# Kernel tuning notes

Hardware: AMD Instinct MI355X
Metric: run time of the kernel (lower is better)

Reference implementation:

```python
import jax, jax.numpy as jnp
import numpy as np

T, B, E, H, V, K = 512, 64, 256, 512, 50000, 50
START, STOP = 0, K - 1  # tags = ['<START>'] + tags + ['<STOP>']


def setup_inputs() -> dict:
    key = jax.random.key(0)
    ks = jax.random.split(key, 13)
    p = lambda k, shape, s=0.02: jax.random.normal(k, shape, jnp.float32) * s
    return {
        'tokens': jax.random.randint(ks[0], (T, B), 0, V, dtype=jnp.int32),
        'embed': p(ks[1], (V, E), 0.1),
        'w_ih_f': p(ks[2], (4 * H, E)), 'w_hh_f': p(ks[3], (4 * H, H)), 'b_f': jnp.zeros((4 * H,), jnp.float32),
        'w_ih_b': p(ks[4], (4 * H, E)), 'w_hh_b': p(ks[5], (4 * H, H)), 'b_b': jnp.zeros((4 * H,), jnp.float32),
        'w_enc': p(ks[6], (H, 2 * H)), 'b_enc': jnp.zeros((H,), jnp.float32),
        'w_out': p(ks[7], (K, H)), 'b_out': jnp.zeros((K,), jnp.float32),
        'trans': p(ks[8], (K, K), 0.1),
    }


def _lstm_dir(x, w_ih, w_hh, b, reverse):
    # x: [T,B,E] -> hidden states [T,B,H]; torch gate order i,f,g,o
    bsz = x.shape[1]
    h_dim = w_hh.shape[1]
    xp = jnp.einsum('tbe,ge->tbg', x, w_ih) + b  # precompute input projections

    def step(carry, xt):
        h, c = carry
        g = xt + h @ w_hh.T
        i, f, gg, o = jnp.split(g, 4, axis=-1)
        c = jax.nn.sigmoid(f) * c + jax.nn.sigmoid(i) * jnp.tanh(gg)
        h = jax.nn.sigmoid(o) * jnp.tanh(c)
        return (h, c), h

    init = (jnp.zeros((bsz, h_dim), x.dtype), jnp.zeros((bsz, h_dim), x.dtype))
    _, hs = jax.lax.scan(step, init, xp, reverse=reverse)
    return hs


def reference(tokens, embed, w_ih_f, w_hh_f, b_f, w_ih_b, w_hh_b, b_b,
              w_enc, b_enc, w_out, b_out, trans):
    x = embed[tokens]  # [T,B,E]
    hf = _lstm_dir(x, w_ih_f, w_hh_f, b_f, reverse=False)
    hb = _lstm_dir(x, w_ih_b, w_hh_b, b_b, reverse=True)
    enc = jnp.concatenate([hf, hb], axis=-1)                      # [T,B,2H]
    states = jnp.tanh(jnp.einsum('tbd,hd->tbh', enc, w_enc) + b_enc)
    emit = jnp.einsum('tbh,kh->tbk', states, w_out) + b_out       # [T,B,K]

    # CRF forward algorithm (log partition). trans[j, i] = score of i -> j.
    NEG = jnp.float32(-10000.0)
    bsz, k = emit.shape[1], emit.shape[2]
    alpha0 = jnp.full((bsz, k), NEG).at[:, START].set(0.0)

    def crf_step(alpha, e_t):
        # scores[b, j, i] = alpha[b, i] + trans[j, i] + emit[b, t, j]
        s = alpha[:, None, :] + trans[None, :, :] + e_t[:, :, None]
        return jax.nn.logsumexp(s, axis=-1), None

    alpha, _ = jax.lax.scan(crf_step, alpha0, emit)
    log_z = jax.nn.logsumexp(alpha + trans[STOP][None, :], axis=-1)  # [B]
    return log_z
```

## Files before the change

### kernel.cpp

```cpp
#include <hip/hip_runtime.h>
#include <stdint.h>

#define T_ 512
#define B_ 64
#define E_ 256
#define H_ 512
#define KT 50

typedef __attribute__((ext_vector_type(8))) short bf16x8;
typedef __attribute__((ext_vector_type(4))) float f32x4;
typedef __attribute__((ext_vector_type(4))) int i32x4;

#define MFMA16(a,b,c) __builtin_amdgcn_mfma_f32_16x16x32_bf16((a),(b),(c),0,0,0)

static __device__ __forceinline__ float bf2f(unsigned short v) {
  unsigned int u = ((unsigned int)v) << 16; float f; __builtin_memcpy(&f, &u, 4); return f;
}
static __device__ __forceinline__ unsigned short f2bf(float f) {
  unsigned int u; __builtin_memcpy(&u, &f, 4);
  u += 0x7fffu + ((u >> 16) & 1u);
  return (unsigned short)(u >> 16);
}
static __device__ __forceinline__ float sigm(float x) { return 1.f / (1.f + __expf(-x)); }
static __device__ __forceinline__ float tanh_(float x) { return 2.f / (1.f + __expf(-2.f * x)) - 1.f; }

static __device__ __forceinline__ unsigned int load_dw_dev(const unsigned int* p) {
  unsigned int v;
  asm volatile("global_load_dword %0, %1, off sc0 sc1\n\ts_waitcnt vmcnt(0)"
               : "=v"(v) : "v"(p) : "memory");
  return v;
}

__global__ void probe_kernel(const unsigned short* __restrict__ e,
                             unsigned int* __restrict__ flag) {
  int lane = threadIdx.x & 63;
  float a = fabsf(bf2f(e[2 * lane]));
  int good = (a >= 1e-8f && a <= 4.0f);
  unsigned long long m = __ballot(good);
  if (threadIdx.x == 0) flag[0] = (__popcll(m) >= 48) ? 1u : 0u;
}

struct CvtArgs { const void* src; unsigned short* dst; int n; };
struct CvtPack { CvtArgs a[11]; };

__global__ __launch_bounds__(256) void convert_kernel(CvtPack p,
                                                      const unsigned int* __restrict__ flag) {
  CvtArgs c = p.a[blockIdx.y];
  int i = (blockIdx.x * 256 + threadIdx.x) * 8;
  if (i >= c.n) return;
  int isbf = *flag;
  if (i + 8 <= c.n) {
    if (isbf) {
      *(i32x4*)(c.dst + i) = *(const i32x4*)((const unsigned short*)c.src + i);
    } else {
      const float* s = (const float*)c.src;
      float4 a0 = *(const float4*)(s + i);
      float4 a1 = *(const float4*)(s + i + 4);
      unsigned short o[8] = {f2bf(a0.x), f2bf(a0.y), f2bf(a0.z), f2bf(a0.w),
                             f2bf(a1.x), f2bf(a1.y), f2bf(a1.z), f2bf(a1.w)};
      *(i32x4*)(c.dst + i) = *(i32x4*)o;
    }
  } else {
    for (int j = 0; j < 8; j++) {
      if (i + j < c.n) {
        c.dst[i + j] = isbf ? ((const unsigned short*)c.src)[i + j]
                            : f2bf(((const float*)c.src)[i + j]);
      }
    }
  }
}

__global__ __launch_bounds__(256) void embed_kernel(
    const int* __restrict__ tokens, const void* __restrict__ embed,
    const unsigned int* __restrict__ flag, unsigned short* __restrict__ x) {
  int tid = threadIdx.x;
  int row = blockIdx.x * 8 + (tid >> 5);
  int l = tid & 31;
  int tok = tokens[row];
  if (*flag) {
    const unsigned short* e = (const unsigned short*)embed;
    *(i32x4*)(x + (size_t)row * E_ + l * 8) =
        *(const i32x4*)(e + (size_t)tok * E_ + l * 8);
  } else {
    const float* e = (const float*)embed + (size_t)tok * E_ + l * 8;
    float4 a0 = *(const float4*)e;
    float4 a1 = *(const float4*)(e + 4);
    unsigned short o[8] = {f2bf(a0.x), f2bf(a0.y), f2bf(a0.z), f2bf(a0.w),
                           f2bf(a1.x), f2bf(a1.y), f2bf(a1.z), f2bf(a1.w)};
    *(i32x4*)(x + (size_t)row * E_ + l * 8) = *(i32x4*)o;
  }
}

__global__ __launch_bounds__(256, 1) void lstm_kernel(
    const unsigned short* __restrict__ whh_f, const unsigned short* __restrict__ wih_f,
    const unsigned short* __restrict__ bias_f,
    const unsigned short* __restrict__ whh_b, const unsigned short* __restrict__ wih_b,
    const unsigned short* __restrict__ bias_b,
    const unsigned short* __restrict__ x,
    unsigned short* __restrict__ hf, unsigned short* __restrict__ hb,
    unsigned int* __restrict__ tags) {
  const int tid = threadIdx.x;
  const int wv = tid >> 6, lane = tid & 63, q = lane >> 4, l15 = lane & 15;
  const int bid = blockIdx.x;
  const int dir = bid & 1;
  const int wg = bid >> 1;
  const int u0 = wg * 16;

  const unsigned short* whh = dir ? whh_b : whh_f;
  const unsigned short* wih = dir ? wih_b : wih_f;
  const unsigned short* bvec = dir ? bias_b : bias_f;
  unsigned short* hbuf = dir ? hb : hf;
  unsigned int* tbase = tags + (size_t)dir * 512;

  bf16x8 afrag[4][6];
#pragma unroll
  for (int mt = 0; mt < 4; mt++) {
    int row = mt * H_ + u0 + l15;
#pragma unroll
    for (int kl = 0; kl < 6; kl++) {
      const unsigned short* p = (kl < 4)
          ? (whh + (size_t)row * H_ + (wv * 4 + kl) * 32 + q * 8)
          : (wih + (size_t)row * E_ + (wv * 2 + (kl - 4)) * 32 + q * 8);
      afrag[mt][kl] = *(const bf16x8*)p;
    }
  }

  const int eb = tid & 63;
  const int uu = tid >> 6;
  float bg[4][4];
#pragma unroll
  for (int s = 0; s < 4; s++) {
    int u = uu + 4 * s;
#pragma unroll
    for (int g = 0; g < 4; g++) bg[s][g] = bf2f(bvec[g * H_ + u0 + u]);
  }
  float cst[4] = {0.f, 0.f, 0.f, 0.f};

  __shared__ float pacc[4][64][66];
  __shared__ __align__(16) unsigned short h_out[64][16];
  __shared__ unsigned int go_word;
  if (tid == 0) go_word = 0;

  for (int step = 0; step < T_; step++) {
    const int t = dir ? (T_ - 1 - step) : step;
    f32x4 acc[4][4];
#pragma unroll
    for (int mt = 0; mt < 4; mt++)
#pragma unroll
      for (int nt = 0; nt < 4; nt++) acc[mt][nt] = (f32x4){0.f, 0.f, 0.f, 0.f};

    {
      const unsigned short* xb = x + (size_t)t * B_ * E_;
#pragma unroll
      for (int kl = 4; kl < 6; kl++) {
        int ec = wv * 2 + (kl - 4);
#pragma unroll
        for (int nt = 0; nt < 4; nt++) {
          int b = nt * 16 + l15;
          bf16x8 bx = *(const bf16x8*)(xb + (size_t)b * E_ + ec * 32 + q * 8);
#pragma unroll
          for (int mt = 0; mt < 4; mt++)
            acc[mt][nt] = MFMA16(afrag[mt][kl], bx, acc[mt][nt]);
        }
      }
    }

    if (step > 0) {
      if (wv == 1) {
        const unsigned int* tp = tbase + (size_t)(lane & 31) * 16;
        for (;;) {
          unsigned int v = load_dw_dev(tp);
          unsigned long long m = __ballot((lane < 32) ? (v >= (unsigned)step) : 1);
          if (m == ~0ULL) break;
          __builtin_amdgcn_s_sleep(1);
        }
        __hip_atomic_store(&go_word, (unsigned int)step, __ATOMIC_RELAXED,
                           __HIP_MEMORY_SCOPE_WORKGROUP);
      } else {
        while (__hip_atomic_load(&go_word, __ATOMIC_RELAXED,
                                 __HIP_MEMORY_SCOPE_WORKGROUP) < (unsigned int)step)
          __builtin_amdgcn_s_sleep(1);
      }
      asm volatile("" ::: "memory");

      const int tprev = dir ? (t + 1) : (t - 1);
      const unsigned int* hD = (const unsigned int*)hbuf + (size_t)tprev * 16384;

      const unsigned int* a0 = hD + ((wv * 4 + 0) * 4 + q) * 256 + l15 * 4;
      const unsigned int* a1 = hD + ((wv * 4 + 1) * 4 + q) * 256 + l15 * 4;
      const unsigned int* a2 = hD + ((wv * 4 + 2) * 4 + q) * 256 + l15 * 4;
      const unsigned int* a3 = hD + ((wv * 4 + 3) * 4 + q) * 256 + l15 * 4;
      i32x4 h00, h01, h02, h03, h10, h11, h12, h13;
      i32x4 h20, h21, h22, h23, h30, h31, h32, h33;
      asm volatile(
          "global_load_dwordx4 %0, %16, off sc0 sc1\n\t"
          "global_load_dwordx4 %1, %16, off offset:1024 sc0 sc1\n\t"
          "global_load_dwordx4 %2, %16, off offset:2048 sc0 sc1\n\t"
          "global_load_dwordx4 %3, %16, off offset:3072 sc0 sc1\n\t"
          "global_load_dwordx4 %4, %17, off sc0 sc1\n\t"
          "global_load_dwordx4 %5, %17, off offset:1024 sc0 sc1\n\t"
          "global_load_dwordx4 %6, %17, off offset:2048 sc0 sc1\n\t"
          "global_load_dwordx4 %7, %17, off offset:3072 sc0 sc1\n\t"
          "global_load_dwordx4 %8, %18, off sc0 sc1\n\t"
          "global_load_dwordx4 %9, %18, off offset:1024 sc0 sc1\n\t"
          "global_load_dwordx4 %10, %18, off offset:2048 sc0 sc1\n\t"
          "global_load_dwordx4 %11, %18, off offset:3072 sc0 sc1\n\t"
          "global_load_dwordx4 %12, %19, off sc0 sc1\n\t"
          "global_load_dwordx4 %13, %19, off offset:1024 sc0 sc1\n\t"
          "global_load_dwordx4 %14, %19, off offset:2048 sc0 sc1\n\t"
          "global_load_dwordx4 %15, %19, off offset:3072 sc0 sc1\n\t"
          "s_waitcnt vmcnt(0)"
          : "=&v"(h00), "=&v"(h01), "=&v"(h02), "=&v"(h03),
            "=&v"(h10), "=&v"(h11), "=&v"(h12), "=&v"(h13),
            "=&v"(h20), "=&v"(h21), "=&v"(h22), "=&v"(h23),
            "=&v"(h30), "=&v"(h31), "=&v"(h32), "=&v"(h33)
          : "v"(a0), "v"(a1), "v"(a2), "v"(a3)
          : "memory");
      i32x4 hr4[16] = {h00, h01, h02, h03, h10, h11, h12, h13,
                       h20, h21, h22, h23, h30, h31, h32, h33};
#pragma unroll
      for (int kl = 0; kl < 4; kl++) {
#pragma unroll
        for (int nt = 0; nt < 4; nt++) {
          bf16x8 bh;
          __builtin_memcpy(&bh, &hr4[kl * 4 + nt], 16);
#pragma unroll
          for (int mt = 0; mt < 4; mt++)
            acc[mt][nt] = MFMA16(afrag[mt][kl], bh, acc[mt][nt]);
        }
      }
    }

    __syncthreads();
#pragma unroll
    for (int mt = 0; mt < 4; mt++)
#pragma unroll
      for (int nt = 0; nt < 4; nt++)
#pragma unroll
        for (int r = 0; r < 4; r++)
          pacc[wv][mt * 16 + q * 4 + r][nt * 16 + l15] = acc[mt][nt][r];
    __syncthreads();

#pragma unroll
    for (int s = 0; s < 4; s++) {
      int u = uu + 4 * s;
      float gi = bg[s][0], gf = bg[s][1], gg = bg[s][2], og = bg[s][3];
#pragma unroll
      for (int w = 0; w < 4; w++) {
        gi += pacc[w][u][eb];
        gf += pacc[w][16 + u][eb];
        gg += pacc[w][32 + u][eb];
        og += pacc[w][48 + u][eb];
      }
      float cn = sigm(gf) * cst[s] + sigm(gi) * tanh_(gg);
      cst[s] = cn;
      h_out[eb][u] = f2bf(sigm(og) * tanh_(cn));
    }
    __syncthreads();

    if (wv == 0) {
      unsigned int* gp = (unsigned int*)hbuf + (size_t)t * 16384 + wg * 512 + lane * 4;
      i32x4 v0 = *(const i32x4*)&h_out[lane][0];
      i32x4 v1 = *(const i32x4*)&h_out[lane][8];
      asm volatile(
          "global_store_dwordx4 %0, %1, off sc0 sc1\n\t"
          "global_store_dwordx4 %0, %2, off offset:1024 sc0 sc1\n\t"
          "s_waitcnt vmcnt(0)"
          :: "v"(gp), "v"(v0), "v"(v1) : "memory");
      if (lane == 0) {
        unsigned int* tp = tbase + (size_t)wg * 16;
        unsigned int tv = (unsigned int)(step + 1);
        asm volatile("global_store_dword %0, %1, off sc0 sc1"
                     :: "v"(tp), "v"(tv) : "memory");
      }
    }
  }
}

__global__ __launch_bounds__(256) void enc_kernel(
    const unsigned short* __restrict__ hf, const unsigned short* __restrict__ hb,
    const unsigned short* __restrict__ w_enc, const unsigned short* __restrict__ b_enc,
    unsigned short* __restrict__ states) {
  const int tid = threadIdx.x;
  const int bm = blockIdx.x, bn = blockIdx.y;
  const int wv = tid >> 6, lane = tid & 63, q = lane >> 4, l15 = lane & 15;
  const int wm = wv >> 1, wn = wv & 1;

  __shared__ __align__(16) unsigned short a_lds[128][72];
  __shared__ __align__(16) unsigned short b_lds[128][72];
  __shared__ __align__(16) unsigned short st_lds[128][136];

  f32x4 acc[4][4];
#pragma unroll
  for (int mt = 0; mt < 4; mt++)
#pragma unroll
    for (int nt = 0; nt < 4; nt++) acc[mt][nt] = (f32x4){0.f, 0.f, 0.f, 0.f};

  for (int c = 0; c < 16; c++) {
    const unsigned short* asrc = (c < 8) ? hf : hb;
    int kof = (c & 7) * 64;
#pragma unroll
    for (int p = 0; p < 4; p++) {
      int u_ = tid + p * 256;
      int r = u_ >> 3, wu = u_ & 7;
      int grow = bm * 128 + r;
      *(i32x4*)&a_lds[r][wu * 8] =
          *(const i32x4*)((const unsigned int*)asrc + (size_t)(grow >> 6) * 16384 +
                          (size_t)((kof >> 3) + wu) * 256 + (grow & 63) * 4);
      *(i32x4*)&b_lds[r][wu * 8] =
          *(const i32x4*)(w_enc + (size_t)(bn * 128 + r) * 1024 + c * 64 + wu * 8);
    }
    __syncthreads();
#pragma unroll
    for (int kk = 0; kk < 64; kk += 32) {
      bf16x8 af[4], bfr[4];
#pragma unroll
      for (int mt = 0; mt < 4; mt++)
        af[mt] = *(const bf16x8*)&a_lds[wm * 64 + mt * 16 + l15][kk + q * 8];
#pragma unroll
      for (int nt = 0; nt < 4; nt++)
        bfr[nt] = *(const bf16x8*)&b_lds[wn * 64 + nt * 16 + l15][kk + q * 8];
#pragma unroll
      for (int mt = 0; mt < 4; mt++)
#pragma unroll
        for (int nt = 0; nt < 4; nt++) acc[mt][nt] = MFMA16(af[mt], bfr[nt], acc[mt][nt]);
    }
    __syncthreads();
  }

  float be[4];
#pragma unroll
  for (int nt = 0; nt < 4; nt++)
    be[nt] = bf2f(b_enc[bn * 128 + wn * 64 + nt * 16 + l15]);
#pragma unroll
  for (int mt = 0; mt < 4; mt++)
#pragma unroll
    for (int nt = 0; nt < 4; nt++)
#pragma unroll
      for (int r = 0; r < 4; r++) {
        float v = tanh_(acc[mt][nt][r] + be[nt]);
        st_lds[wm * 64 + mt * 16 + q * 4 + r][wn * 64 + nt * 16 + l15] = f2bf(v);
      }
  __syncthreads();
#pragma unroll
  for (int p = 0; p < 8; p++) {
    int u_ = tid + p * 256;
    int r = u_ >> 4, w = u_ & 15;
    *(i32x4*)(states + (size_t)(bm * 128 + r) * H_ + bn * 128 + w * 8) =
        *(const i32x4*)&st_lds[r][w * 8];
  }
}

__global__ __launch_bounds__(256) void emit_kernel(
    const unsigned short* __restrict__ states, const unsigned short* __restrict__ w_out,
    const unsigned short* __restrict__ b_out, float* __restrict__ emit) {
  const int tid = threadIdx.x;
  const int bm = blockIdx.x;
  const int wv = tid >> 6, lane = tid & 63, q = lane >> 4, l15 = lane & 15;
  const int wm = wv >> 1, wn = wv & 1;

  __shared__ __align__(16) unsigned short wo_lds[64][520];
  __shared__ __align__(16) unsigned short a_lds[128][72];

#pragma unroll
  for (int p = 0; p < 16; p++) {
    int u = tid + p * 256;
    int r = u >> 6, wu = u & 63;
    i32x4 v = {0, 0, 0, 0};
    if (r < KT) v = *(const i32x4*)(w_out + (size_t)r * H_ + wu * 8);
    *(i32x4*)&wo_lds[r][wu * 8] = v;
  }

  f32x4 acc[4][2];
#pragma unroll
  for (int mt = 0; mt < 4; mt++)
#pragma unroll
    for (int nt = 0; nt < 2; nt++) acc[mt][nt] = (f32x4){0.f, 0.f, 0.f, 0.f};

  for (int c = 0; c < 8; c++) {
    __syncthreads();
#pragma unroll
    for (int p = 0; p < 4; p++) {
      int u = tid + p * 256;
      int r = u >> 3, wu = u & 7;
      *(i32x4*)&a_lds[r][wu * 8] =
          *(const i32x4*)(states + (size_t)(bm * 128 + r) * H_ + c * 64 + wu * 8);
    }
    __syncthreads();
#pragma unroll
    for (int kk = 0; kk < 64; kk += 32) {
      bf16x8 af[4], bfr[2];
#pragma unroll
      for (int mt = 0; mt < 4; mt++)
        af[mt] = *(const bf16x8*)&a_lds[wm * 64 + mt * 16 + l15][kk + q * 8];
#pragma unroll
      for (int nt = 0; nt < 2; nt++)
        bfr[nt] = *(const bf16x8*)&wo_lds[wn * 32 + nt * 16 + l15][c * 64 + kk + q * 8];
#pragma unroll
      for (int mt = 0; mt < 4; mt++)
#pragma unroll
        for (int nt = 0; nt < 2; nt++) acc[mt][nt] = MFMA16(af[mt], bfr[nt], acc[mt][nt]);
    }
  }

  float bo[2];
#pragma unroll
  for (int nt = 0; nt < 2; nt++) {
    int n = wn * 32 + nt * 16 + l15;
    bo[nt] = (n < KT) ? bf2f(b_out[n]) : 0.f;
  }
#pragma unroll
  for (int mt = 0; mt < 4; mt++)
#pragma unroll
    for (int nt = 0; nt < 2; nt++) {
      int n = wn * 32 + nt * 16 + l15;
      if (n < KT) {
#pragma unroll
        for (int r = 0; r < 4; r++) {
          int m = bm * 128 + wm * 64 + mt * 16 + q * 4 + r;
          emit[(size_t)m * KT + n] = acc[mt][nt][r] + bo[nt];
        }
      }
    }
}

__global__ __launch_bounds__(256) void crf_kernel(
    const float* __restrict__ emit, const unsigned short* __restrict__ trans,
    const unsigned int* __restrict__ flag, void* __restrict__ out) {
  const int tid = threadIdx.x;
  const int wv = tid >> 6, lane = tid & 63;
  const int b = blockIdx.x * 4 + wv;
  const int jj = (lane < KT) ? lane : (KT - 1);

  float tr[KT];
  float mj = -1e30f;
#pragma unroll
  for (int i = 0; i < KT; i++) {
    tr[i] = bf2f(trans[jj * KT + i]);
    mj = fmaxf(mj, tr[i]);
  }
  float et[KT];
#pragma unroll
  for (int i = 0; i < KT; i++) et[i] = __expf(tr[i] - mj);
  float tr_stop = bf2f(trans[(KT - 1) * KT + jj]);

  float alpha = (lane == 0) ? 0.f : -1e30f;
  float e_next = emit[(size_t)b * KT + jj];

  for (int t = 0; t < T_; t++) {
    float e_cur = e_next;
    if (t < T_ - 1) e_next = emit[((size_t)(t + 1) * B_ + b) * KT + jj];
    float M = alpha;
#pragma unroll
    for (int off = 32; off; off >>= 1) M = fmaxf(M, __shfl_xor(M, off, 64));
    float p = __expf(alpha - M);
    float s = 0.f;
#pragma unroll
    for (int i = 0; i < KT; i++) {
      float pi = __uint_as_float(__builtin_amdgcn_readlane(__float_as_uint(p), i));
      s = __builtin_fmaf(et[i], pi, s);
    }
    float an = e_cur + mj + M + __logf(s);
    alpha = (lane < KT) ? an : -1e30f;
  }

  float v = (lane < KT) ? (alpha + tr_stop) : -1e30f;
  float M2 = v;
#pragma unroll
  for (int off = 32; off; off >>= 1) M2 = fmaxf(M2, __shfl_xor(M2, off, 64));
  float s2 = (lane < KT) ? __expf(v - M2) : 0.f;
#pragma unroll
  for (int off = 32; off; off >>= 1) s2 += __shfl_xor(s2, off, 64);
  float lz = M2 + __logf(s2);
  if (lane == 0) {
    if (*flag) ((unsigned short*)out)[b] = f2bf(lz);
    else ((float*)out)[b] = lz;
  }
}

extern "C" void kernel_launch(void* const* d_in, const int* in_sizes, int n_in,
                              void* d_out, int out_size, void* d_ws, size_t ws_size,
                              hipStream_t stream) {
  const int* tokens = (const int*)d_in[0];
  const void* embed = d_in[1];
  const void* wih_f = d_in[2];
  const void* whh_f = d_in[3];
  const void* b_f = d_in[4];
  const void* wih_b = d_in[5];
  const void* whh_b = d_in[6];
  const void* b_b = d_in[7];
  const void* w_enc = d_in[8];
  const void* b_enc = d_in[9];
  const void* w_out = d_in[10];
  const void* b_out = d_in[11];
  const void* trans = d_in[12];

  char* ws = (char*)d_ws;
  unsigned int* tags = (unsigned int*)ws;
  unsigned int* pflag = (unsigned int*)(ws + 262144);
  unsigned short* xbuf = (unsigned short*)(ws + 262400);
  unsigned short* hf = (unsigned short*)(ws + 17039616);
  unsigned short* hb = (unsigned short*)(ws + 50594048);
  unsigned short* states = (unsigned short*)(ws + 84148480);
  float* emit = (float*)(ws + 117702912);
  unsigned short* canon = (unsigned short*)(ws + 124256512);

  unsigned short* c_wih_f = canon + 0;
  unsigned short* c_whh_f = canon + 524288;
  unsigned short* c_b_f   = canon + 1572864;
  unsigned short* c_wih_b = canon + 1574912;
  unsigned short* c_whh_b = canon + 2099200;
  unsigned short* c_b_b   = canon + 3147776;
  unsigned short* c_w_enc = canon + 3149824;
  unsigned short* c_b_enc = canon + 3674112;
  unsigned short* c_w_out = canon + 3674624;
  unsigned short* c_b_out = canon + 3700224;
  unsigned short* c_trans = canon + 3700352;

  hipMemsetAsync(tags, 0, 4096, stream);
  probe_kernel<<<1, 64, 0, stream>>>((const unsigned short*)embed, pflag);

  CvtPack pk;
  pk.a[0]  = {wih_f, c_wih_f, 524288};
  pk.a[1]  = {whh_f, c_whh_f, 1048576};
  pk.a[2]  = {b_f,   c_b_f,   2048};
  pk.a[3]  = {wih_b, c_wih_b, 524288};
  pk.a[4]  = {whh_b, c_whh_b, 1048576};
  pk.a[5]  = {b_b,   c_b_b,   2048};
  pk.a[6]  = {w_enc, c_w_enc, 524288};
  pk.a[7]  = {b_enc, c_b_enc, 512};
  pk.a[8]  = {w_out, c_w_out, 25600};
  pk.a[9]  = {b_out, c_b_out, 50};
  pk.a[10] = {trans, c_trans, 2500};
  convert_kernel<<<dim3(512, 11), 256, 0, stream>>>(pk, pflag);

  embed_kernel<<<(T_ * B_) / 8, 256, 0, stream>>>(tokens, embed, pflag, xbuf);
  lstm_kernel<<<64, 256, 0, stream>>>(c_whh_f, c_wih_f, c_b_f,
                                      c_whh_b, c_wih_b, c_b_b,
                                      xbuf, hf, hb, tags);
  enc_kernel<<<dim3(256, 4), 256, 0, stream>>>(hf, hb, c_w_enc, c_b_enc, states);
  emit_kernel<<<256, 256, 0, stream>>>(states, c_w_out, c_b_out, emit);
  crf_kernel<<<16, 256, 0, stream>>>(emit, c_trans, pflag, d_out);
}
```

Baseline: 2.789 ms.

## Pin each LSTM direction to one XCD and use L2-coherent sync

Launches 512 workgroups and reads the XCC_ID hardware register so that the first two XCDs to fill 32 workgroups each take one LSTM direction, and all other workgroups exit. A runtime probe then checks whether a store with sc0 only is visible to another workgroup in the same direction. If it is, the per-step hidden-state exchange and tag polling use sc0 loads and stores that stay in the shared L2 instead of sc1 system-coherent traffic. This is meant to cut inter-workgroup sync latency, at the cost of relying on undocumented dispatch behaviour and spinning workgroups during role assignment.

```diff
diff --git a/kernel.cpp b/kernel.cpp
--- a/kernel.cpp
+++ b/kernel.cpp
@@ -24,10 +24,14 @@
 static __device__ __forceinline__ float sigm(float x) { return 1.f / (1.f + __expf(-x)); }
 static __device__ __forceinline__ float tanh_(float x) { return 2.f / (1.f + __expf(-2.f * x)) - 1.f; }
 
-static __device__ __forceinline__ unsigned int load_dw_dev(const unsigned int* p) {
+static __device__ __forceinline__ unsigned int load_tag(const unsigned int* p, bool mall) {
   unsigned int v;
-  asm volatile("global_load_dword %0, %1, off sc0 sc1\n\ts_waitcnt vmcnt(0)"
-               : "=v"(v) : "v"(p) : "memory");
+  if (mall)
+    asm volatile("global_load_dword %0, %1, off sc0 sc1\n\ts_waitcnt vmcnt(0)"
+                 : "=v"(v) : "v"(p) : "memory");
+  else
+    asm volatile("global_load_dword %0, %1, off sc0\n\ts_waitcnt vmcnt(0)"
+                 : "=v"(v) : "v"(p) : "memory");
   return v;
 }
 
@@ -98,13 +102,54 @@
     const unsigned short* __restrict__ bias_b,
     const unsigned short* __restrict__ x,
     unsigned short* __restrict__ hf, unsigned short* __restrict__ hb,
-    unsigned int* __restrict__ tags) {
+    unsigned int* __restrict__ tags, unsigned int* __restrict__ ctrl) {
   const int tid = threadIdx.x;
+
+  __shared__ float pacc[4][64][66];
+  __shared__ __align__(16) unsigned short h_out[64][16];
+  __shared__ unsigned int lds_misc[3136];
+
+  if (tid == 0) {
+    unsigned int xcc;
+    asm volatile("s_getreg_b32 %0, hwreg(HW_REG_XCC_ID)" : "=s"(xcc));
+    xcc &= 15;
+    unsigned int slot = __hip_atomic_fetch_add(&ctrl[xcc], 1u, __ATOMIC_RELAXED,
+                                               __HIP_MEMORY_SCOPE_AGENT);
+    unsigned int role;
+    if (slot == 31) {
+      unsigned int r = __hip_atomic_fetch_add(&ctrl[16], 1u, __ATOMIC_RELAXED,
+                                              __HIP_MEMORY_SCOPE_AGENT);
+      role = (r < 2) ? (r + 1) : 3;
+      __hip_atomic_store(&ctrl[32 + xcc], role, __ATOMIC_RELAXED,
+                         __HIP_MEMORY_SCOPE_AGENT);
+      asm volatile("s_waitcnt vmcnt(0)" ::: "memory");
+      __hip_atomic_fetch_add(&ctrl[17], 1u, __ATOMIC_RELAXED,
+                             __HIP_MEMORY_SCOPE_AGENT);
+    } else {
+      for (;;) {
+        role = __hip_atomic_load(&ctrl[32 + xcc], __ATOMIC_RELAXED,
+                                 __HIP_MEMORY_SCOPE_AGENT);
+        if (role) break;
+        if (__hip_atomic_load(&ctrl[17], __ATOMIC_RELAXED,
+                              __HIP_MEMORY_SCOPE_AGENT) >= 2) {
+          role = __hip_atomic_load(&ctrl[32 + xcc], __ATOMIC_RELAXED,
+                                   __HIP_MEMORY_SCOPE_AGENT);
+          if (role == 0) role = 3;
+          break;
+        }
+        __builtin_amdgcn_s_sleep(8);
+      }
+    }
+    lds_misc[1] = role; lds_misc[2] = slot; lds_misc[0] = 0;
+  }
+  __syncthreads();
+  const unsigned int role = lds_misc[1];
+  const unsigned int wg = lds_misc[2];
+  if (role > 2 || wg >= 32) return;
+  const int dir = (int)role - 1;
+
   const int wv = tid >> 6, lane = tid & 63, q = lane >> 4, l15 = lane & 15;
-  const int bid = blockIdx.x;
-  const int dir = bid & 1;
-  const int wg = bid >> 1;
-  const int u0 = wg * 16;
+  const int u0 = (int)wg * 16;
 
   const unsigned short* whh = dir ? whh_b : whh_f;
   const unsigned short* wih = dir ? wih_b : wih_f;
@@ -136,10 +181,33 @@
   }
   float cst[4] = {0.f, 0.f, 0.f, 0.f};
 
-  __shared__ float pacc[4][64][66];
-  __shared__ __align__(16) unsigned short h_out[64][16];
-  __shared__ unsigned int go_word;
-  if (tid == 0) go_word = 0;
+  if (tid == 0) {
+    unsigned int* tw = ctrl + 64 + 32 * dir;
+    unsigned int* vw = ctrl + 128 + 32 * dir;
+    unsigned int sent = 0x5EED0001u + (unsigned)dir;
+    if (wg == 0) {
+      asm volatile("global_store_dword %0, %1, off sc0" :: "v"(tw), "v"(sent) : "memory");
+    } else if (wg == 1) {
+      unsigned int verdict = 1;
+      for (int it = 0; it < 4096; it++) {
+        unsigned int v;
+        asm volatile("global_load_dword %0, %1, off sc0\n\ts_waitcnt vmcnt(0)"
+                     : "=v"(v) : "v"(tw) : "memory");
+        if (v == sent) { verdict = 2; break; }
+        __builtin_amdgcn_s_sleep(1);
+      }
+      asm volatile("global_store_dword %0, %1, off sc0 sc1" :: "v"(vw), "v"(verdict) : "memory");
+    }
+    for (;;) {
+      unsigned int v;
+      asm volatile("global_load_dword %0, %1, off sc0 sc1\n\ts_waitcnt vmcnt(0)"
+                   : "=v"(v) : "v"(vw) : "memory");
+      if (v) { lds_misc[3] = v; break; }
+      __builtin_amdgcn_s_sleep(8);
+    }
+  }
+  __syncthreads();
+  const bool mall = (lds_misc[3] == 1u);
 
   for (int step = 0; step < T_; step++) {
     const int t = dir ? (T_ - 1 - step) : step;
@@ -169,15 +237,15 @@
       if (wv == 1) {
         const unsigned int* tp = tbase + (size_t)(lane & 31) * 16;
         for (;;) {
-          unsigned int v = load_dw_dev(tp);
+          unsigned int v = load_tag(tp, mall);
           unsigned long long m = __ballot((lane < 32) ? (v >= (unsigned)step) : 1);
           if (m == ~0ULL) break;
           __builtin_amdgcn_s_sleep(1);
         }
-        __hip_atomic_store(&go_word, (unsigned int)step, __ATOMIC_RELAXED,
+        __hip_atomic_store(&lds_misc[0], (unsigned int)step, __ATOMIC_RELAXED,
                            __HIP_MEMORY_SCOPE_WORKGROUP);
       } else {
-        while (__hip_atomic_load(&go_word, __ATOMIC_RELAXED,
+        while (__hip_atomic_load(&lds_misc[0], __ATOMIC_RELAXED,
                                  __HIP_MEMORY_SCOPE_WORKGROUP) < (unsigned int)step)
           __builtin_amdgcn_s_sleep(1);
       }
@@ -192,30 +260,57 @@
       const unsigned int* a3 = hD + ((wv * 4 + 3) * 4 + q) * 256 + l15 * 4;
       i32x4 h00, h01, h02, h03, h10, h11, h12, h13;
       i32x4 h20, h21, h22, h23, h30, h31, h32, h33;
-      asm volatile(
-          "global_load_dwordx4 %0, %16, off sc0 sc1\n\t"
-          "global_load_dwordx4 %1, %16, off offset:1024 sc0 sc1\n\t"
-          "global_load_dwordx4 %2, %16, off offset:2048 sc0 sc1\n\t"
-          "global_load_dwordx4 %3, %16, off offset:3072 sc0 sc1\n\t"
-          "global_load_dwordx4 %4, %17, off sc0 sc1\n\t"
-          "global_load_dwordx4 %5, %17, off offset:1024 sc0 sc1\n\t"
-          "global_load_dwordx4 %6, %17, off offset:2048 sc0 sc1\n\t"
-          "global_load_dwordx4 %7, %17, off offset:3072 sc0 sc1\n\t"
-          "global_load_dwordx4 %8, %18, off sc0 sc1\n\t"
-          "global_load_dwordx4 %9, %18, off offset:1024 sc0 sc1\n\t"
-          "global_load_dwordx4 %10, %18, off offset:2048 sc0 sc1\n\t"
-          "global_load_dwordx4 %11, %18, off offset:3072 sc0 sc1\n\t"
-          "global_load_dwordx4 %12, %19, off sc0 sc1\n\t"
-          "global_load_dwordx4 %13, %19, off offset:1024 sc0 sc1\n\t"
-          "global_load_dwordx4 %14, %19, off offset:2048 sc0 sc1\n\t"
-          "global_load_dwordx4 %15, %19, off offset:3072 sc0 sc1\n\t"
-          "s_waitcnt vmcnt(0)"
-          : "=&v"(h00), "=&v"(h01), "=&v"(h02), "=&v"(h03),
-            "=&v"(h10), "=&v"(h11), "=&v"(h12), "=&v"(h13),
-            "=&v"(h20), "=&v"(h21), "=&v"(h22), "=&v"(h23),
-            "=&v"(h30), "=&v"(h31), "=&v"(h32), "=&v"(h33)
-          : "v"(a0), "v"(a1), "v"(a2), "v"(a3)
-          : "memory");
+      if (mall) {
+        asm volatile(
+            "global_load_dwordx4 %0, %16, off sc0 sc1\n\t"
+            "global_load_dwordx4 %1, %16, off offset:1024 sc0 sc1\n\t"
+            "global_load_dwordx4 %2, %16, off offset:2048 sc0 sc1\n\t"
+            "global_load_dwordx4 %3, %16, off offset:3072 sc0 sc1\n\t"
+            "global_load_dwordx4 %4, %17, off sc0 sc1\n\t"
+            "global_load_dwordx4 %5, %17, off offset:1024 sc0 sc1\n\t"
+            "global_load_dwordx4 %6, %17, off offset:2048 sc0 sc1\n\t"
+            "global_load_dwordx4 %7, %17, off offset:3072 sc0 sc1\n\t"
+            "global_load_dwordx4 %8, %18, off sc0 sc1\n\t"
+            "global_load_dwordx4 %9, %18, off offset:1024 sc0 sc1\n\t"
+            "global_load_dwordx4 %10, %18, off offset:2048 sc0 sc1\n\t"
+            "global_load_dwordx4 %11, %18, off offset:3072 sc0 sc1\n\t"
+            "global_load_dwordx4 %12, %19, off sc0 sc1\n\t"
+            "global_load_dwordx4 %13, %19, off offset:1024 sc0 sc1\n\t"
+            "global_load_dwordx4 %14, %19, off offset:2048 sc0 sc1\n\t"
+            "global_load_dwordx4 %15, %19, off offset:3072 sc0 sc1\n\t"
+            "s_waitcnt vmcnt(0)"
+            : "=&v"(h00), "=&v"(h01), "=&v"(h02), "=&v"(h03),
+              "=&v"(h10), "=&v"(h11), "=&v"(h12), "=&v"(h13),
+              "=&v"(h20), "=&v"(h21), "=&v"(h22), "=&v"(h23),
+              "=&v"(h30), "=&v"(h31), "=&v"(h32), "=&v"(h33)
+            : "v"(a0), "v"(a1), "v"(a2), "v"(a3)
+            : "memory");
+      } else {
+        asm volatile(
+            "global_load_dwordx4 %0, %16, off sc0\n\t"
+            "global_load_dwordx4 %1, %16, off offset:1024 sc0\n\t"
+            "global_load_dwordx4 %2, %16, off offset:2048 sc0\n\t"
+            "global_load_dwordx4 %3, %16, off offset:3072 sc0\n\t"
+            "global_load_dwordx4 %4, %17, off sc0\n\t"
+            "global_load_dwordx4 %5, %17, off offset:1024 sc0\n\t"
+            "global_load_dwordx4 %6, %17, off offset:2048 sc0\n\t"
+            "global_load_dwordx4 %7, %17, off offset:3072 sc0\n\t"
+            "global_load_dwordx4 %8, %18, off sc0\n\t"
+            "global_load_dwordx4 %9, %18, off offset:1024 sc0\n\t"
+            "global_load_dwordx4 %10, %18, off offset:2048 sc0\n\t"
+            "global_load_dwordx4 %11, %18, off offset:3072 sc0\n\t"
+            "global_load_dwordx4 %12, %19, off sc0\n\t"
+            "global_load_dwordx4 %13, %19, off offset:1024 sc0\n\t"
+            "global_load_dwordx4 %14, %19, off offset:2048 sc0\n\t"
+            "global_load_dwordx4 %15, %19, off offset:3072 sc0\n\t"
+            "s_waitcnt vmcnt(0)"
+            : "=&v"(h00), "=&v"(h01), "=&v"(h02), "=&v"(h03),
+              "=&v"(h10), "=&v"(h11), "=&v"(h12), "=&v"(h13),
+              "=&v"(h20), "=&v"(h21), "=&v"(h22), "=&v"(h23),
+              "=&v"(h30), "=&v"(h31), "=&v"(h32), "=&v"(h33)
+            : "v"(a0), "v"(a1), "v"(a2), "v"(a3)
+            : "memory");
+      }
       i32x4 hr4[16] = {h00, h01, h02, h03, h10, h11, h12, h13,
                        h20, h21, h22, h23, h30, h31, h32, h33};
 #pragma unroll
@@ -262,16 +357,26 @@
       unsigned int* gp = (unsigned int*)hbuf + (size_t)t * 16384 + wg * 512 + lane * 4;
       i32x4 v0 = *(const i32x4*)&h_out[lane][0];
       i32x4 v1 = *(const i32x4*)&h_out[lane][8];
-      asm volatile(
-          "global_store_dwordx4 %0, %1, off sc0 sc1\n\t"
-          "global_store_dwordx4 %0, %2, off offset:1024 sc0 sc1\n\t"
-          "s_waitcnt vmcnt(0)"
-          :: "v"(gp), "v"(v0), "v"(v1) : "memory");
+      if (mall) {
+        asm volatile(
+            "global_store_dwordx4 %0, %1, off sc0 sc1\n\t"
+            "global_store_dwordx4 %0, %2, off offset:1024 sc0 sc1\n\t"
+            "s_waitcnt vmcnt(0)"
+            :: "v"(gp), "v"(v0), "v"(v1) : "memory");
+      } else {
+        asm volatile(
+            "global_store_dwordx4 %0, %1, off sc0\n\t"
+            "global_store_dwordx4 %0, %2, off offset:1024 sc0\n\t"
+            "s_waitcnt vmcnt(0)"
+            :: "v"(gp), "v"(v0), "v"(v1) : "memory");
+      }
       if (lane == 0) {
         unsigned int* tp = tbase + (size_t)wg * 16;
         unsigned int tv = (unsigned int)(step + 1);
-        asm volatile("global_store_dword %0, %1, off sc0 sc1"
-                     :: "v"(tp), "v"(tv) : "memory");
+        if (mall)
+          asm volatile("global_store_dword %0, %1, off sc0 sc1" :: "v"(tp), "v"(tv) : "memory");
+        else
+          asm volatile("global_store_dword %0, %1, off sc0" :: "v"(tp), "v"(tv) : "memory");
       }
     }
   }
@@ -497,6 +602,7 @@
 
   char* ws = (char*)d_ws;
   unsigned int* tags = (unsigned int*)ws;
+  unsigned int* ctrl = (unsigned int*)(ws + 4096);
   unsigned int* pflag = (unsigned int*)(ws + 262144);
   unsigned short* xbuf = (unsigned short*)(ws + 262400);
   unsigned short* hf = (unsigned short*)(ws + 17039616);
@@ -517,7 +623,7 @@
   unsigned short* c_b_out = canon + 3700224;
   unsigned short* c_trans = canon + 3700352;
 
-  hipMemsetAsync(tags, 0, 4096, stream);
+  hipMemsetAsync(ws, 0, 5120, stream);
   probe_kernel<<<1, 64, 0, stream>>>((const unsigned short*)embed, pflag);
 
   CvtPack pk;
@@ -535,9 +641,9 @@
   convert_kernel<<<dim3(512, 11), 256, 0, stream>>>(pk, pflag);
 
   embed_kernel<<<(T_ * B_) / 8, 256, 0, stream>>>(tokens, embed, pflag, xbuf);
-  lstm_kernel<<<64, 256, 0, stream>>>(c_whh_f, c_wih_f, c_b_f,
-                                      c_whh_b, c_wih_b, c_b_b,
-                                      xbuf, hf, hb, tags);
+  lstm_kernel<<<512, 256, 0, stream>>>(c_whh_f, c_wih_f, c_b_f,
+                                       c_whh_b, c_wih_b, c_b_b,
+                                       xbuf, hf, hb, tags, ctrl);
   enc_kernel<<<dim3(256, 4), 256, 0, stream>>>(hf, hb, c_w_enc, c_b_enc, states);
   emit_kernel<<<256, 256, 0, stream>>>(states, c_w_out, c_b_out, emit);
   crf_kernel<<<16, 256, 0, stream>>>(emit, c_trans, pflag, d_out);
```

Result: slower. 3.106 ms (+11.4%).
